# Optimization experiments

Measured on AMD Instinct MI355X. Metric: run time of the kernel, lower is better.

The kernel has to match this reference:

```python
import jax, jax.numpy as jnp
import numpy as np

R, B, F, H, C = 32, 2048, 512, 1024, 100  # n_rules, batch, n_fea, 2*n_fea, n_cls


def setup_inputs() -> dict:
    key = jax.random.key(0)
    ks = jax.random.split(key, 10)
    sc = lambda k, shape, fan: (jax.random.normal(k, shape, jnp.float32) / np.float32(np.sqrt(fan)))
    return {
        "data": jax.random.normal(ks[0], (B, F), jnp.float32),
        "proto": jax.random.normal(ks[1], (R, F), jnp.float32),
        "var": jax.random.uniform(ks[2], (R, F), jnp.float32, 0.5, 1.5),
        "fs_w1": sc(ks[3], (F, H), F), "fs_b1": jnp.zeros((H,), jnp.float32),
        "fs_w2": sc(ks[4], (H, F), H), "fs_b2": jnp.zeros((F,), jnp.float32),
        "fs_w3": sc(ks[5], (F, 1), F), "fs_b3": jnp.zeros((1,), jnp.float32),
        "cq_w1": sc(ks[6], (R, F, H), F), "cq_b1": jnp.zeros((R, H), jnp.float32),
        "cq_w2": sc(ks[7], (R, H, F), H), "cq_b2": jnp.zeros((R, F), jnp.float32),
        "cq_w3": sc(ks[8], (R, F, C), F), "cq_b3": jnp.zeros((R, C), jnp.float32),
        "is_train": 1,
    }


def reference(data, proto, var, fs_w1, fs_b1, fs_w2, fs_b2, fs_w3, fs_b3,
              cq_w1, cq_b1, cq_w2, cq_b2, cq_w3, cq_b3, is_train):
    # Gaussian fuzzy membership per rule: [R, B, F]
    fuzzy = jnp.exp(-(data[None, :, :] - proto[:, None, :]) ** 2
                    / (2.0 * var[:, None, :] ** 2))
    # shared fire-strength MLP applied per rule
    h = jax.nn.relu(jnp.einsum('rbf,fh->rbh', fuzzy, fs_w1) + fs_b1)
    h = jax.nn.relu(jnp.einsum('rbh,hf->rbf', h, fs_w2) + fs_b2)
    fs_logits = (jnp.einsum('rbf,fo->rbo', h, fs_w3) + fs_b3)[..., 0]  # [R, B]
    fire = jax.nn.softmax(fs_logits.T, axis=1)  # [B, R], softmax over rules
    # per-rule consequent MLPs on raw data (grouped GEMMs)
    g = jax.nn.relu(jnp.einsum('bf,rfh->rbh', data, cq_w1) + cq_b1[:, None, :])
    g = jax.nn.relu(jnp.einsum('rbh,rhf->rbf', g, cq_w2) + cq_b2[:, None, :])
    logits = jnp.einsum('rbf,rfc->rbc', g, cq_w3) + cq_b3[:, None, :]  # [R, B, C]
    # softmax-weighted expert sum, then class softmax
    out = jnp.einsum('br,rbc->bc', fire, logits)  # [B, C]
    return jax.nn.softmax(out, axis=1)
```

## Files before the change

### kernel.cpp

```cpp
#include <hip/hip_runtime.h>

typedef __attribute__((ext_vector_type(8))) short short8;
typedef __attribute__((ext_vector_type(4))) float f32x4;

__device__ __forceinline__ unsigned short f2bf(float f) {
    union { float f; unsigned u; } v; v.f = f;
    unsigned r = v.u + 0x7FFFu + ((v.u >> 16) & 1u);
    return (unsigned short)(r >> 16);
}

__global__ __launch_bounds__(256)
void transpose_kernel(const float* __restrict__ X, unsigned short* __restrict__ Y,
                      int K, int N, int Np) {
    __shared__ float tile[32][33];
    int g = blockIdx.z;
    const float* Xg = X + (long)g * K * N;
    unsigned short* Yg = Y + (long)g * Np * K;
    int k0 = blockIdx.x * 32, n0 = blockIdx.y * 32;
    int tx = threadIdx.x & 31, ty = threadIdx.x >> 5;
#pragma unroll
    for (int i = 0; i < 4; ++i) {
        int kk = ty + i * 8;
        int n = n0 + tx;
        tile[kk][tx] = (n < N) ? Xg[(long)(k0 + kk) * N + n] : 0.0f;
    }
    __syncthreads();
#pragma unroll
    for (int i = 0; i < 4; ++i) {
        int nn = ty + i * 8;
        Yg[(long)(n0 + nn) * K + k0 + tx] = f2bf(tile[tx][nn]);
    }
}

__global__ __launch_bounds__(256)
void fuzzy_kernel(const float* __restrict__ data, const float* __restrict__ proto,
                  const float* __restrict__ var, unsigned short* __restrict__ fuzzy,
                  unsigned short* __restrict__ data_bf) {
    int t = threadIdx.x;
    int rb = blockIdx.x * 2 + (t >> 7);
    int r = rb >> 11, b = rb & 2047;
    int f = (t & 127) * 4;
    float4 d = *(const float4*)(data + (long)b * 512 + f);
    float4 p = *(const float4*)(proto + (long)r * 512 + f);
    float4 w = *(const float4*)(var + (long)r * 512 + f);
    ushort4 o;
    float x;
    x = d.x - p.x; o.x = f2bf(__expf(-(x * x) / (2.f * w.x * w.x)));
    x = d.y - p.y; o.y = f2bf(__expf(-(x * x) / (2.f * w.y * w.y)));
    x = d.z - p.z; o.z = f2bf(__expf(-(x * x) / (2.f * w.z * w.z)));
    x = d.w - p.w; o.w = f2bf(__expf(-(x * x) / (2.f * w.w * w.w)));
    *(ushort4*)(fuzzy + (long)rb * 512 + f) = o;
    if (r == 0) {
        ushort4 od;
        od.x = f2bf(d.x); od.y = f2bf(d.y); od.z = f2bf(d.z); od.w = f2bf(d.w);
        *(ushort4*)(data_bf + (long)b * 512 + f) = od;
    }
}

#define RING_WAIT_BARRIER(n)                                        \
    asm volatile("s_waitcnt vmcnt(" #n ")" ::: "memory");           \
    __builtin_amdgcn_sched_barrier(0);                              \
    __builtin_amdgcn_s_barrier();                                   \
    __builtin_amdgcn_sched_barrier(0);

template<int EPI, bool RELU>
__global__ __launch_bounds__(512, 2)
void gemm256_kernel(const unsigned short* __restrict__ A,
                    const unsigned short* __restrict__ Bt,
                    const float* __restrict__ bias,
                    void* __restrict__ Cptr,
                    const float* __restrict__ w3,
                    float* __restrict__ fslog,
                    int nM, int nN, int K,
                    long sAg, long sBg, long sCg, int sBiasG) {
    unsigned tot = gridDim.x, bid = blockIdx.x;
    unsigned sw = (bid & 7u) * (tot >> 3) + (bid >> 3);
    unsigned pg = (unsigned)(nM * nN);
    unsigned g = sw / pg;
    unsigned rem = sw - g * pg;
    const int m0 = (int)(rem / (unsigned)nN) * 256;
    const int n0 = (int)(rem % (unsigned)nN) * 256;
    const int N = nN * 256;
    A += (long)g * sAg; Bt += (long)g * sBg; bias += (long)g * sBiasG;

    __shared__ __align__(16) unsigned short lds[8][8192];

    const int tid = threadIdx.x;
    const int lane = tid & 63;
    const int w = tid >> 6;
    const int wm = w >> 2, wn = w & 3;
    const int r16 = lane & 15, kg = lane >> 4;

    f32x4 acc[8][4];
#pragma unroll
    for (int i = 0; i < 8; ++i)
#pragma unroll
        for (int j = 0; j < 4; ++j) {
            f32x4 z = {0.f, 0.f, 0.f, 0.f};
            acc[i][j] = z;
        }

    const int nsteps = K >> 5;

    auto STAGE = [&](int slot, int kt) {
        const int k0 = kt << 5;
#pragma unroll
        for (int j = 0; j < 2; ++j) {
            int f = j * 512 + tid;
            int row = f >> 2, sl = f & 3;
            int kk = (sl ^ ((row >> 1) & 3)) << 3;
            const unsigned short* ga = A + (long)(m0 + row) * K + k0 + kk;
            __builtin_amdgcn_global_load_lds(
                (const __attribute__((address_space(1))) void*)ga,
                (__attribute__((address_space(3))) void*)(&lds[slot][0] + (j * 512 + w * 64) * 8),
                16, 0, 0);
            const unsigned short* gb = Bt + (long)(n0 + row) * K + k0 + kk;
            __builtin_amdgcn_global_load_lds(
                (const __attribute__((address_space(1))) void*)gb,
                (__attribute__((address_space(3))) void*)(&lds[4 + slot][0] + (j * 512 + w * 64) * 8),
                16, 0, 0);
        }
    };

    auto COMPUTE = [&](int slot) {
        short8 aF[8], bF[4];
#pragma unroll
        for (int mt = 0; mt < 8; ++mt) {
            int R = wm * 128 + mt * 16 + r16;
            aF[mt] = *(const short8*)(&lds[slot][0] + R * 32 + ((kg ^ ((R >> 1) & 3)) << 3));
        }
#pragma unroll
        for (int nt = 0; nt < 4; ++nt) {
            int R = wn * 64 + nt * 16 + r16;
            bF[nt] = *(const short8*)(&lds[4 + slot][0] + R * 32 + ((kg ^ ((R >> 1) & 3)) << 3));
        }
        __builtin_amdgcn_s_setprio(1);
#pragma unroll
        for (int mt = 0; mt < 8; ++mt)
#pragma unroll
            for (int nt = 0; nt < 4; ++nt)
                acc[mt][nt] = __builtin_amdgcn_mfma_f32_16x16x32_bf16(
                    aF[mt], bF[nt], acc[mt][nt], 0, 0, 0);
        __builtin_amdgcn_s_setprio(0);
        asm volatile("" ::: "memory");
        __builtin_amdgcn_s_barrier();
        __builtin_amdgcn_sched_barrier(0);
    };

    STAGE(0, 0); STAGE(1, 1); STAGE(2, 2);
    for (int t = 0; t <= nsteps - 3; ++t) {
        if (t + 3 < nsteps) STAGE((t + 3) & 3, t + 3);
        RING_WAIT_BARRIER(8);
        COMPUTE(t & 3);
    }
    { RING_WAIT_BARRIER(4); COMPUTE((nsteps - 2) & 3); }
    { RING_WAIT_BARRIER(0); COMPUTE((nsteps - 1) & 3); }

    if constexpr (EPI == 1) {
        float w3v[4], bv[4];
#pragma unroll
        for (int nt = 0; nt < 4; ++nt) {
            int col = n0 + wn * 64 + nt * 16 + r16;
            w3v[nt] = w3[col];
            bv[nt] = bias[col];
        }
#pragma unroll
        for (int mt = 0; mt < 8; ++mt) {
#pragma unroll
            for (int j = 0; j < 4; ++j) {
                float p = 0.f;
#pragma unroll
                for (int nt = 0; nt < 4; ++nt) {
                    float v = acc[mt][nt][j] + bv[nt];
                    if (RELU) v = fmaxf(v, 0.f);
                    p += v * w3v[nt];
                }
                p += __shfl_xor(p, 1, 64);
                p += __shfl_xor(p, 2, 64);
                p += __shfl_xor(p, 4, 64);
                p += __shfl_xor(p, 8, 64);
                if (r16 == 0) {
                    int row = m0 + wm * 128 + mt * 16 + kg * 4 + j;
                    atomicAdd(&fslog[row], p);
                }
            }
        }
    } else {
        unsigned short* ldsC = &lds[0][0];
        float bv[4];
#pragma unroll
        for (int nt = 0; nt < 4; ++nt) bv[nt] = bias[n0 + wn * 64 + nt * 16 + r16];
#pragma unroll
        for (int mt = 0; mt < 8; ++mt) {
            int rr = wm * 128 + mt * 16 + kg * 4;
#pragma unroll
            for (int nt = 0; nt < 4; ++nt) {
                int cc = wn * 64 + nt * 16 + r16;
#pragma unroll
                for (int j = 0; j < 4; ++j) {
                    float v = acc[mt][nt][j] + bv[nt];
                    if (RELU) v = fmaxf(v, 0.f);
                    ldsC[(rr + j) * 256 + cc] = f2bf(v);
                }
            }
        }
        __syncthreads();
        unsigned short* Cg = (unsigned short*)Cptr + (long)g * sCg;
#pragma unroll
        for (int rnd = 0; rnd < 16; ++rnd) {
            int idx = rnd * 512 + tid;
            int row = idx >> 5;
            int c8 = idx & 31;
            short8 vv = *(const short8*)(ldsC + row * 256 + c8 * 8);
            *(short8*)(Cg + (long)(m0 + row) * N + n0 + c8 * 8) = vv;
        }
    }
}

template<int EPI, bool RELU>
__global__ __launch_bounds__(256, 2)
void gemm_kernel(const unsigned short* __restrict__ A,
                 const unsigned short* __restrict__ Bt,
                 const float* __restrict__ bias,
                 void* __restrict__ Cptr,
                 int nM, int nN, int K,
                 long sAg, long sBg, long sCg, int sBiasG, int biasN,
                 const float* __restrict__ fire, float* __restrict__ mix, int r0) {
    unsigned tot = gridDim.x;
    unsigned bid = blockIdx.x;
    unsigned sw = (tot & 7u) == 0 ? (bid & 7u) * (tot >> 3) + (bid >> 3) : bid;
    unsigned pg = (unsigned)nM * (unsigned)nN;
    unsigned g = sw / pg;
    unsigned rem = sw - g * pg;
    unsigned mt_ = rem / (unsigned)nN;
    unsigned nt_ = rem - mt_ * (unsigned)nN;
    const int N = nN * 128;
    A += (long)g * sAg;
    Bt += (long)g * sBg;
    bias += (long)g * sBiasG;
    const int m0 = (int)mt_ * 128;
    const int n0 = (int)nt_ * 128;

    __shared__ __align__(16) unsigned short ldsA[128 * 32];
    __shared__ __align__(16) unsigned short ldsB[128 * 32];

    const int tid = threadIdx.x;
    const int lane = tid & 63;
    const int w = tid >> 6;
    const int wm = w >> 1, wn = w & 1;
    const int r16 = lane & 15, kg = lane >> 4;

    f32x4 acc[4][4];
#pragma unroll
    for (int i = 0; i < 4; ++i)
#pragma unroll
        for (int j = 0; j < 4; ++j) {
            f32x4 z = {0.f, 0.f, 0.f, 0.f};
            acc[i][j] = z;
        }

    for (int k0 = 0; k0 < K; k0 += 32) {
#pragma unroll
        for (int j = 0; j < 2; ++j) {
            int t = j * 256 + tid;
            int row = t >> 2, kc = (t & 3) * 8;
            const unsigned short* ga = A + (long)(m0 + row) * K + k0 + kc;
            __builtin_amdgcn_global_load_lds(
                (const __attribute__((address_space(1))) void*)ga,
                (__attribute__((address_space(3))) void*)(ldsA + (j * 256 + w * 64) * 8),
                16, 0, 0);
            const unsigned short* gb = Bt + (long)(n0 + row) * K + k0 + kc;
            __builtin_amdgcn_global_load_lds(
                (const __attribute__((address_space(1))) void*)gb,
                (__attribute__((address_space(3))) void*)(ldsB + (j * 256 + w * 64) * 8),
                16, 0, 0);
        }
        __syncthreads();
        short8 aF[4], bF[4];
#pragma unroll
        for (int mt = 0; mt < 4; ++mt)
            aF[mt] = *(const short8*)(ldsA + (wm * 64 + mt * 16 + r16) * 32 + kg * 8);
#pragma unroll
        for (int nt = 0; nt < 4; ++nt)
            bF[nt] = *(const short8*)(ldsB + (wn * 64 + nt * 16 + r16) * 32 + kg * 8);
#pragma unroll
        for (int mt = 0; mt < 4; ++mt)
#pragma unroll
            for (int nt = 0; nt < 4; ++nt)
                acc[mt][nt] = __builtin_amdgcn_mfma_f32_16x16x32_bf16(
                    aF[mt], bF[nt], acc[mt][nt], 0, 0, 0);
        __syncthreads();
    }

    if constexpr (EPI == 3) {
        float bv[4];
#pragma unroll
        for (int nt = 0; nt < 4; ++nt) {
            int col = n0 + wn * 64 + nt * 16 + r16;
            bv[nt] = (col < biasN) ? bias[col] : 0.f;
        }
#pragma unroll
        for (int mt = 0; mt < 4; ++mt) {
#pragma unroll
            for (int j = 0; j < 4; ++j) {
                int row = m0 + wm * 64 + mt * 16 + kg * 4 + j;
                float f = fire[row * 32 + r0 + (int)g];
#pragma unroll
                for (int nt = 0; nt < 4; ++nt) {
                    int col = n0 + wn * 64 + nt * 16 + r16;
                    float v = acc[mt][nt][j] + bv[nt];
                    atomicAdd(&mix[row * 128 + col], f * v);
                }
            }
        }
    } else {
#pragma unroll
        for (int nt = 0; nt < 4; ++nt) {
            int col = n0 + wn * 64 + nt * 16 + r16;
            float bv = (col < biasN) ? bias[col] : 0.f;
#pragma unroll
            for (int mt = 0; mt < 4; ++mt) {
#pragma unroll
                for (int j = 0; j < 4; ++j) {
                    int row = m0 + wm * 64 + mt * 16 + kg * 4 + j;
                    float v = acc[mt][nt][j] + bv;
                    if (RELU) v = fmaxf(v, 0.f);
                    ((float*)Cptr)[(long)g * sCg + (long)row * N + col] = v;
                }
            }
        }
    }
}

__global__ __launch_bounds__(256)
void fire_kernel(const float* __restrict__ fslog, float* __restrict__ fire) {
    int b = blockIdx.x * 256 + threadIdx.x;
    float v[32];
    float mx = -1e30f;
#pragma unroll
    for (int r = 0; r < 32; ++r) { v[r] = fslog[r * 2048 + b]; mx = fmaxf(mx, v[r]); }
    float s = 0.f;
#pragma unroll
    for (int r = 0; r < 32; ++r) { v[r] = __expf(v[r] - mx); s += v[r]; }
    float inv = 1.f / s;
#pragma unroll
    for (int r = 0; r < 32; ++r) fire[b * 32 + r] = v[r] * inv;
}

__global__ __launch_bounds__(128)
void softmax_out_kernel(const float* __restrict__ mix, float* __restrict__ out) {
    int b = blockIdx.x, c = threadIdx.x;
    __shared__ float redm[2], reds[2];
    float val = (c < 100) ? mix[b * 128 + c] : -1e30f;
    float m = val;
#pragma unroll
    for (int off = 32; off; off >>= 1) m = fmaxf(m, __shfl_xor(m, off, 64));
    int lane = c & 63, wv = c >> 6;
    if (lane == 0) redm[wv] = m;
    __syncthreads();
    m = fmaxf(redm[0], redm[1]);
    float e = (c < 100) ? __expf(val - m) : 0.f;
    float s = e;
#pragma unroll
    for (int off = 32; off; off >>= 1) s += __shfl_xor(s, off, 64);
    if (lane == 0) reds[wv] = s;
    __syncthreads();
    s = reds[0] + reds[1];
    if (c < 100) out[b * 100 + c] = e / s;
}

extern "C" void kernel_launch(void* const* d_in, const int* in_sizes, int n_in,
                              void* d_out, int out_size, void* d_ws, size_t ws_size,
                              hipStream_t stream) {
    const float* data  = (const float*)d_in[0];
    const float* proto = (const float*)d_in[1];
    const float* var   = (const float*)d_in[2];
    const float* fs_w1 = (const float*)d_in[3];
    const float* fs_b1 = (const float*)d_in[4];
    const float* fs_w2 = (const float*)d_in[5];
    const float* fs_b2 = (const float*)d_in[6];
    const float* fs_w3 = (const float*)d_in[7];
    const float* cq_w1 = (const float*)d_in[9];
    const float* cq_b1 = (const float*)d_in[10];
    const float* cq_w2 = (const float*)d_in[11];
    const float* cq_b2 = (const float*)d_in[12];
    const float* cq_w3 = (const float*)d_in[13];
    const float* cq_b3 = (const float*)d_in[14];
    float* out = (float*)d_out;

    const size_t H1SZ   = (size_t)65536 * 1024 * 2;
    const size_t FUZZSZ = (size_t)65536 * 512 * 2;
    char* ws = (char*)d_ws;
    size_t off = 0;
    auto take = [&](size_t bytes) { char* p = ws + off; off += bytes; return p; };
    unsigned short* data_bf = (unsigned short*)take(2097152);
    unsigned short* w1t     = (unsigned short*)take(1048576);
    unsigned short* w2t     = (unsigned short*)take(1048576);
    float*          fslog   = (float*)take(262144);
    float*          fire    = (float*)take(262144);
    float*          mix     = (float*)take(1048576);
    unsigned short* h1      = (unsigned short*)take(H1SZ);
    unsigned short* fuzzy   = (unsigned short*)take(FUZZSZ);
    unsigned short* g1   = h1;
    unsigned short* cW1t = h1 + (size_t)33554432;
    unsigned short* cW2t = h1 + (size_t)50331648;
    unsigned short* g2   = fuzzy;
    unsigned short* cW3t = fuzzy + (size_t)16777216;
    const int p2r = 16;

    transpose_kernel<<<dim3(16, 32, 1), 256, 0, stream>>>(fs_w1, w1t, 512, 1024, 1024);
    transpose_kernel<<<dim3(32, 16, 1), 256, 0, stream>>>(fs_w2, w2t, 1024, 512, 512);
    hipMemsetAsync(fslog, 0, 262144, stream);
    hipMemsetAsync(mix, 0, 1048576, stream);

    fuzzy_kernel<<<32768, 256, 0, stream>>>(data, proto, var, fuzzy, data_bf);
    gemm256_kernel<0, true><<<256 * 4, 512, 0, stream>>>(
        fuzzy, w1t, fs_b1, h1, nullptr, nullptr, 256, 4, 512, 0, 0, 0, 0);
    gemm256_kernel<1, true><<<256 * 2, 512, 0, stream>>>(
        h1, w2t, fs_b2, nullptr, fs_w3, fslog, 256, 2, 1024, 0, 0, 0, 0);
    fire_kernel<<<8, 256, 0, stream>>>(fslog, fire);

    transpose_kernel<<<dim3(16, 32, 32), 256, 0, stream>>>(cq_w1, cW1t, 512, 1024, 1024);
    transpose_kernel<<<dim3(32, 16, 32), 256, 0, stream>>>(cq_w2, cW2t, 1024, 512, 512);
    transpose_kernel<<<dim3(16, 4, 32), 256, 0, stream>>>(cq_w3, cW3t, 512, 100, 128);

    for (int ch = 0; ch < 32 / p2r; ++ch) {
        const int r0 = ch * p2r;
        gemm256_kernel<0, true><<<8 * 4 * p2r, 512, 0, stream>>>(
            data_bf, cW1t + (long)r0 * 1024 * 512, cq_b1 + (long)r0 * 1024, g1,
            nullptr, nullptr,
            8, 4, 512, 0, (long)1024 * 512, (long)2048 * 1024, 1024);
        gemm256_kernel<0, true><<<8 * 2 * p2r, 512, 0, stream>>>(
            g1, cW2t + (long)r0 * 512 * 1024, cq_b2 + (long)r0 * 512, g2,
            nullptr, nullptr,
            8, 2, 1024, (long)2048 * 1024, (long)512 * 1024, (long)2048 * 512, 512);
        gemm_kernel<3, false><<<16 * 1 * p2r, 256, 0, stream>>>(
            g2, cW3t + (long)r0 * 128 * 512, cq_b3 + (long)r0 * 100, nullptr,
            16, 1, 512, (long)2048 * 512, (long)128 * 512, 0, 100, 100,
            fire, mix, r0);
    }
    softmax_out_kernel<<<2048, 128, 0, stream>>>(mix, out);
}
```

Before: 513.1 us.

## Use swizzled 128x128 GEMM kernel for fire-strength MLP layers

Adds a gemm128 kernel that loads from global memory straight into LDS using an XOR-swizzled k-chunk layout, to avoid LDS bank conflicts on the fragment reads. It supports a bf16 LDS-staged store epilogue, a fused w3 dot-product epilogue that accumulates fire-strength logits atomically, and the rule-mixing epilogue. The two fire-strength GEMMs move from the 256-tile, 512-thread kernel to this 128-tile kernel with four times as many blocks, and the per-rule final GEMM switches to it as well. The smaller tiles reuse less data per block and do more atomic adds in the w3 epilogue, in exchange for more parallelism and conflict-free LDS reads.

```diff
diff --git a/kernel.cpp b/kernel.cpp
--- a/kernel.cpp
+++ b/kernel.cpp
@@ -57,6 +57,166 @@
     }
 }
 
+template<int EPI, bool RELU>
+__global__ __launch_bounds__(256, 2)
+void gemm128_kernel(const unsigned short* __restrict__ A,
+                    const unsigned short* __restrict__ Bt,
+                    const float* __restrict__ bias,
+                    void* __restrict__ Cptr,
+                    const float* __restrict__ w3,
+                    float* __restrict__ fsl_or_mix,
+                    const float* __restrict__ fire,
+                    int nM, int nN, int K,
+                    long sAg, long sBg, long sCg, int sBiasG, int biasN, int r0) {
+    unsigned tot = gridDim.x, bid = blockIdx.x;
+    unsigned sw = (tot & 7u) == 0 ? (bid & 7u) * (tot >> 3) + (bid >> 3) : bid;
+    unsigned pg = (unsigned)nM * (unsigned)nN;
+    unsigned g = sw / pg;
+    unsigned rem = sw - g * pg;
+    const int m0 = (int)(rem / (unsigned)nN) * 128;
+    const int n0 = (int)(rem % (unsigned)nN) * 128;
+    const int N = nN * 128;
+    A += (long)g * sAg; Bt += (long)g * sBg; bias += (long)g * sBiasG;
+
+    __shared__ __align__(16) unsigned short ldsU[128 * 128];
+    unsigned short* ldsA = ldsU;
+    unsigned short* ldsB = ldsU + 4096;
+
+    const int tid = threadIdx.x;
+    const int lane = tid & 63;
+    const int w = tid >> 6;
+    const int wm = w >> 1, wn = w & 1;
+    const int r16 = lane & 15, kg = lane >> 4;
+
+    f32x4 acc[4][4];
+#pragma unroll
+    for (int i = 0; i < 4; ++i)
+#pragma unroll
+        for (int j = 0; j < 4; ++j) {
+            f32x4 z = {0.f, 0.f, 0.f, 0.f};
+            acc[i][j] = z;
+        }
+
+    for (int k0 = 0; k0 < K; k0 += 32) {
+#pragma unroll
+        for (int j = 0; j < 2; ++j) {
+            int t = j * 256 + tid;
+            int row = t >> 2, sl = t & 3;
+            int kc = (sl ^ ((row >> 1) & 3)) << 3;
+            const unsigned short* ga = A + (long)(m0 + row) * K + k0 + kc;
+            __builtin_amdgcn_global_load_lds(
+                (const __attribute__((address_space(1))) void*)ga,
+                (__attribute__((address_space(3))) void*)(ldsA + (j * 256 + tid) * 8),
+                16, 0, 0);
+            const unsigned short* gb = Bt + (long)(n0 + row) * K + k0 + kc;
+            __builtin_amdgcn_global_load_lds(
+                (const __attribute__((address_space(1))) void*)gb,
+                (__attribute__((address_space(3))) void*)(ldsB + (j * 256 + tid) * 8),
+                16, 0, 0);
+        }
+        __syncthreads();
+        short8 aF[4], bF[4];
+#pragma unroll
+        for (int mt = 0; mt < 4; ++mt) {
+            int R = wm * 64 + mt * 16 + r16;
+            aF[mt] = *(const short8*)(ldsA + R * 32 + ((kg ^ ((R >> 1) & 3)) << 3));
+        }
+#pragma unroll
+        for (int nt = 0; nt < 4; ++nt) {
+            int R = wn * 64 + nt * 16 + r16;
+            bF[nt] = *(const short8*)(ldsB + R * 32 + ((kg ^ ((R >> 1) & 3)) << 3));
+        }
+#pragma unroll
+        for (int mt = 0; mt < 4; ++mt)
+#pragma unroll
+            for (int nt = 0; nt < 4; ++nt)
+                acc[mt][nt] = __builtin_amdgcn_mfma_f32_16x16x32_bf16(
+                    aF[mt], bF[nt], acc[mt][nt], 0, 0, 0);
+        __syncthreads();
+    }
+
+    if constexpr (EPI == 1) {
+        float w3v[4], bv[4];
+#pragma unroll
+        for (int nt = 0; nt < 4; ++nt) {
+            int col = n0 + wn * 64 + nt * 16 + r16;
+            w3v[nt] = w3[col];
+            bv[nt] = bias[col];
+        }
+#pragma unroll
+        for (int mt = 0; mt < 4; ++mt) {
+#pragma unroll
+            for (int j = 0; j < 4; ++j) {
+                float p = 0.f;
+#pragma unroll
+                for (int nt = 0; nt < 4; ++nt) {
+                    float v = acc[mt][nt][j] + bv[nt];
+                    if (RELU) v = fmaxf(v, 0.f);
+                    p += v * w3v[nt];
+                }
+                p += __shfl_xor(p, 1, 64);
+                p += __shfl_xor(p, 2, 64);
+                p += __shfl_xor(p, 4, 64);
+                p += __shfl_xor(p, 8, 64);
+                if (r16 == 0) {
+                    int row = m0 + wm * 64 + mt * 16 + kg * 4 + j;
+                    atomicAdd(&fsl_or_mix[row], p);
+                }
+            }
+        }
+    } else if constexpr (EPI == 3) {
+        float bv[4];
+#pragma unroll
+        for (int nt = 0; nt < 4; ++nt) {
+            int col = n0 + wn * 64 + nt * 16 + r16;
+            bv[nt] = (col < biasN) ? bias[col] : 0.f;
+        }
+#pragma unroll
+        for (int mt = 0; mt < 4; ++mt) {
+#pragma unroll
+            for (int j = 0; j < 4; ++j) {
+                int row = m0 + wm * 64 + mt * 16 + kg * 4 + j;
+                float f = fire[row * 32 + r0 + (int)g];
+#pragma unroll
+                for (int nt = 0; nt < 4; ++nt) {
+                    int col = n0 + wn * 64 + nt * 16 + r16;
+                    atomicAdd(&fsl_or_mix[row * 128 + col], f * (acc[mt][nt][j] + bv[nt]));
+                }
+            }
+        }
+    } else {
+        float bv[4];
+#pragma unroll
+        for (int nt = 0; nt < 4; ++nt) {
+            int col = n0 + wn * 64 + nt * 16 + r16;
+            bv[nt] = (col < biasN) ? bias[col] : 0.f;
+        }
+#pragma unroll
+        for (int mt = 0; mt < 4; ++mt) {
+            int rl = wm * 64 + mt * 16 + kg * 4;
+#pragma unroll
+            for (int nt = 0; nt < 4; ++nt) {
+                int cc = wn * 64 + nt * 16 + r16;
+#pragma unroll
+                for (int j = 0; j < 4; ++j) {
+                    float v = acc[mt][nt][j] + bv[nt];
+                    if (RELU) v = fmaxf(v, 0.f);
+                    ldsU[(rl + j) * 128 + cc] = f2bf(v);
+                }
+            }
+        }
+        __syncthreads();
+        unsigned short* Cg = (unsigned short*)Cptr + (long)g * sCg;
+#pragma unroll
+        for (int rnd = 0; rnd < 8; ++rnd) {
+            int idx = rnd * 256 + tid;
+            int row = idx >> 4, c8 = idx & 15;
+            short8 vv = *(const short8*)(ldsU + row * 128 + c8 * 8);
+            *(short8*)(Cg + (long)(m0 + row) * N + n0 + c8 * 8) = vv;
+        }
+    }
+}
+
 #define RING_WAIT_BARRIER(n)                                        \
     asm volatile("s_waitcnt vmcnt(" #n ")" ::: "memory");           \
     __builtin_amdgcn_sched_barrier(0);                              \
@@ -217,121 +377,6 @@
     }
 }
 
-template<int EPI, bool RELU>
-__global__ __launch_bounds__(256, 2)
-void gemm_kernel(const unsigned short* __restrict__ A,
-                 const unsigned short* __restrict__ Bt,
-                 const float* __restrict__ bias,
-                 void* __restrict__ Cptr,
-                 int nM, int nN, int K,
-                 long sAg, long sBg, long sCg, int sBiasG, int biasN,
-                 const float* __restrict__ fire, float* __restrict__ mix, int r0) {
-    unsigned tot = gridDim.x;
-    unsigned bid = blockIdx.x;
-    unsigned sw = (tot & 7u) == 0 ? (bid & 7u) * (tot >> 3) + (bid >> 3) : bid;
-    unsigned pg = (unsigned)nM * (unsigned)nN;
-    unsigned g = sw / pg;
-    unsigned rem = sw - g * pg;
-    unsigned mt_ = rem / (unsigned)nN;
-    unsigned nt_ = rem - mt_ * (unsigned)nN;
-    const int N = nN * 128;
-    A += (long)g * sAg;
-    Bt += (long)g * sBg;
-    bias += (long)g * sBiasG;
-    const int m0 = (int)mt_ * 128;
-    const int n0 = (int)nt_ * 128;
-
-    __shared__ __align__(16) unsigned short ldsA[128 * 32];
-    __shared__ __align__(16) unsigned short ldsB[128 * 32];
-
-    const int tid = threadIdx.x;
-    const int lane = tid & 63;
-    const int w = tid >> 6;
-    const int wm = w >> 1, wn = w & 1;
-    const int r16 = lane & 15, kg = lane >> 4;
-
-    f32x4 acc[4][4];
-#pragma unroll
-    for (int i = 0; i < 4; ++i)
-#pragma unroll
-        for (int j = 0; j < 4; ++j) {
-            f32x4 z = {0.f, 0.f, 0.f, 0.f};
-            acc[i][j] = z;
-        }
-
-    for (int k0 = 0; k0 < K; k0 += 32) {
-#pragma unroll
-        for (int j = 0; j < 2; ++j) {
-            int t = j * 256 + tid;
-            int row = t >> 2, kc = (t & 3) * 8;
-            const unsigned short* ga = A + (long)(m0 + row) * K + k0 + kc;
-            __builtin_amdgcn_global_load_lds(
-                (const __attribute__((address_space(1))) void*)ga,
-                (__attribute__((address_space(3))) void*)(ldsA + (j * 256 + w * 64) * 8),
-                16, 0, 0);
-            const unsigned short* gb = Bt + (long)(n0 + row) * K + k0 + kc;
-            __builtin_amdgcn_global_load_lds(
-                (const __attribute__((address_space(1))) void*)gb,
-                (__attribute__((address_space(3))) void*)(ldsB + (j * 256 + w * 64) * 8),
-                16, 0, 0);
-        }
-        __syncthreads();
-        short8 aF[4], bF[4];
-#pragma unroll
-        for (int mt = 0; mt < 4; ++mt)
-            aF[mt] = *(const short8*)(ldsA + (wm * 64 + mt * 16 + r16) * 32 + kg * 8);
-#pragma unroll
-        for (int nt = 0; nt < 4; ++nt)
-            bF[nt] = *(const short8*)(ldsB + (wn * 64 + nt * 16 + r16) * 32 + kg * 8);
-#pragma unroll
-        for (int mt = 0; mt < 4; ++mt)
-#pragma unroll
-            for (int nt = 0; nt < 4; ++nt)
-                acc[mt][nt] = __builtin_amdgcn_mfma_f32_16x16x32_bf16(
-                    aF[mt], bF[nt], acc[mt][nt], 0, 0, 0);
-        __syncthreads();
-    }
-
-    if constexpr (EPI == 3) {
-        float bv[4];
-#pragma unroll
-        for (int nt = 0; nt < 4; ++nt) {
-            int col = n0 + wn * 64 + nt * 16 + r16;
-            bv[nt] = (col < biasN) ? bias[col] : 0.f;
-        }
-#pragma unroll
-        for (int mt = 0; mt < 4; ++mt) {
-#pragma unroll
-            for (int j = 0; j < 4; ++j) {
-                int row = m0 + wm * 64 + mt * 16 + kg * 4 + j;
-                float f = fire[row * 32 + r0 + (int)g];
-#pragma unroll
-                for (int nt = 0; nt < 4; ++nt) {
-                    int col = n0 + wn * 64 + nt * 16 + r16;
-                    float v = acc[mt][nt][j] + bv[nt];
-                    atomicAdd(&mix[row * 128 + col], f * v);
-                }
-            }
-        }
-    } else {
-#pragma unroll
-        for (int nt = 0; nt < 4; ++nt) {
-            int col = n0 + wn * 64 + nt * 16 + r16;
-            float bv = (col < biasN) ? bias[col] : 0.f;
-#pragma unroll
-            for (int mt = 0; mt < 4; ++mt) {
-#pragma unroll
-                for (int j = 0; j < 4; ++j) {
-                    int row = m0 + wm * 64 + mt * 16 + kg * 4 + j;
-                    float v = acc[mt][nt][j] + bv;
-                    if (RELU) v = fmaxf(v, 0.f);
-                    ((float*)Cptr)[(long)g * sCg + (long)row * N + col] = v;
-                }
-            }
-        }
-    }
-}
-
 __global__ __launch_bounds__(256)
 void fire_kernel(const float* __restrict__ fslog, float* __restrict__ fire) {
     int b = blockIdx.x * 256 + threadIdx.x;
@@ -414,10 +459,12 @@
     hipMemsetAsync(mix, 0, 1048576, stream);
 
     fuzzy_kernel<<<32768, 256, 0, stream>>>(data, proto, var, fuzzy, data_bf);
-    gemm256_kernel<0, true><<<256 * 4, 512, 0, stream>>>(
-        fuzzy, w1t, fs_b1, h1, nullptr, nullptr, 256, 4, 512, 0, 0, 0, 0);
-    gemm256_kernel<1, true><<<256 * 2, 512, 0, stream>>>(
-        h1, w2t, fs_b2, nullptr, fs_w3, fslog, 256, 2, 1024, 0, 0, 0, 0);
+    gemm128_kernel<0, true><<<512 * 8, 256, 0, stream>>>(
+        fuzzy, w1t, fs_b1, h1, nullptr, nullptr, nullptr,
+        512, 8, 512, 0, 0, 0, 0, 1024, 0);
+    gemm128_kernel<1, true><<<512 * 4, 256, 0, stream>>>(
+        h1, w2t, fs_b2, nullptr, fs_w3, fslog, nullptr,
+        512, 4, 1024, 0, 0, 0, 0, 512, 0);
     fire_kernel<<<8, 256, 0, stream>>>(fslog, fire);
 
     transpose_kernel<<<dim3(16, 32, 32), 256, 0, stream>>>(cq_w1, cW1t, 512, 1024, 1024);
@@ -434,10 +481,10 @@
             g1, cW2t + (long)r0 * 512 * 1024, cq_b2 + (long)r0 * 512, g2,
             nullptr, nullptr,
             8, 2, 1024, (long)2048 * 1024, (long)512 * 1024, (long)2048 * 512, 512);
-        gemm_kernel<3, false><<<16 * 1 * p2r, 256, 0, stream>>>(
+        gemm128_kernel<3, false><<<16 * 1 * p2r, 256, 0, stream>>>(
             g2, cW3t + (long)r0 * 128 * 512, cq_b3 + (long)r0 * 100, nullptr,
-            16, 1, 512, (long)2048 * 512, (long)128 * 512, 0, 100, 100,
-            fire, mix, r0);
+            nullptr, mix, fire,
+            16, 1, 512, (long)2048 * 512, (long)128 * 512, 0, 100, 100, r0);
     }
     softmax_out_kernel<<<2048, 128, 0, stream>>>(mix, out);
 }
```

New measurement: 520.1 us. No clear change (+1.4%).
